# Performance work log

Hardware: AMD Instinct MI355X
Metric: run time of the kernel (lower is better)

Reference implementation:

```python
import jax, jax.numpy as jnp
import numpy as np

N_NODES = 100000
N_EDGES = 1600000
EPS = 1e-5
ALPHA = 0.01  # leaky relu slope


def gcn_conv(x, src, dst, W, b, n_nodes):
    """PyG GCNConv: h = W x, add self-loops, out = D^-1/2 (A+I) D^-1/2 h + b."""
    h = x @ W  # [N, d_out]
    # add self loops
    loop = jnp.arange(n_nodes, dtype=src.dtype)
    s = jnp.concatenate([src, loop])
    d = jnp.concatenate([dst, loop])
    # symmetric normalization: deg computed at destination over A + I
    deg = jax.ops.segment_sum(jnp.ones_like(d, dtype=h.dtype), d, num_segments=n_nodes)
    dinv = jnp.where(deg > 0, jax.lax.rsqrt(deg), 0.0)
    norm = dinv[s] * dinv[d]  # [E+N]
    msg = h[s] * norm[:, None]  # gather + scale (memory bound)
    out = jax.ops.segment_sum(msg, d, num_segments=n_nodes)
    return out + b


def batch_norm(x, gamma, beta):
    mu = jnp.mean(x, axis=0)
    var = jnp.var(x, axis=0)
    return (x - mu) * jax.lax.rsqrt(var + EPS) * gamma + beta


def setup_inputs() -> dict:
    key = jax.random.key(0)
    ks = jax.random.split(key, 6)
    emb = jax.random.normal(ks[0], (N_NODES, 64), dtype=jnp.float32)
    edge_index = jax.random.randint(ks[1], (2, N_EDGES), 0, N_NODES, dtype=jnp.int32)
    W1 = jax.random.normal(ks[2], (64, 128), dtype=jnp.float32) * 0.05
    W2 = jax.random.normal(ks[3], (128, 256), dtype=jnp.float32) * 0.05
    Wf = jax.random.normal(ks[4], (256, 256), dtype=jnp.float32) * 0.05
    return {
        "embeddings": emb, "edge_index": edge_index,
        "W1": W1, "b1": jnp.zeros((128,), jnp.float32),
        "g1": jnp.ones((128,), jnp.float32), "beta1": jnp.zeros((128,), jnp.float32),
        "W2": W2, "b2": jnp.zeros((256,), jnp.float32),
        "g2": jnp.ones((256,), jnp.float32), "beta2": jnp.zeros((256,), jnp.float32),
        "Wf": Wf, "bf": jnp.zeros((256,), jnp.float32),
    }


def reference(embeddings, edge_index, W1, b1, g1, beta1, W2, b2, g2, beta2, Wf, bf):
    src, dst = edge_index[0], edge_index[1]
    x = gcn_conv(embeddings, src, dst, W1, b1, N_NODES)
    x = batch_norm(x, g1, beta1)
    x = jnp.where(x >= 0, x, ALPHA * x)  # leaky relu; dropout = identity (eval)
    x = gcn_conv(x, src, dst, W2, b2, N_NODES)
    x = batch_norm(x, g2, beta2)
    x = jnp.where(x >= 0, x, ALPHA * x)
    return x @ Wf + bf
```

## Files before the change

### kernel.cpp

```cpp
#include <hip/hip_runtime.h>

#define NN 100000
#define NE 1600000
constexpr float EPS_BN = 1e-5f;
constexpr float ALPHA = 0.01f;
constexpr int GBN = 128;
constexpr int NBUCK = (NN + 127) / 128;
constexpr int GA = 128;
constexpr int EPB = NE / GA;

typedef __attribute__((ext_vector_type(8))) short short8;
typedef __attribute__((ext_vector_type(4))) float f32x4;

__device__ __forceinline__ float bfu2f(uint lo16) {
    union { uint i; float f; } v; v.i = lo16 << 16; return v.f;
}
__device__ __forceinline__ float bfhi2f(uint u) {
    union { uint i; float f; } v; v.i = u & 0xffff0000u; return v.f;
}
__device__ __forceinline__ ushort f2bf(float f) {
    union { float f; uint i; } v; v.f = f;
    return (ushort)((v.i + 0x7fffu + ((v.i >> 16) & 1u)) >> 16);
}

__global__ __launch_bounds__(256) void k_bhist(const int* __restrict__ dstv, int* __restrict__ bcnt) {
    __shared__ int hist[NBUCK];
    for (int i = threadIdx.x; i < NBUCK; i += 256) hist[i] = 0;
    __syncthreads();
    int base = blockIdx.x * EPB;
    for (int i = threadIdx.x; i < EPB; i += 256)
        atomicAdd(&hist[dstv[base + i] >> 7], 1);
    __syncthreads();
    for (int i = threadIdx.x; i < NBUCK; i += 256)
        bcnt[blockIdx.x * NBUCK + i] = hist[i];
}

__global__ __launch_bounds__(1024) void k_bscan(const int* __restrict__ bcnt,
                                                int* __restrict__ gcur, int* __restrict__ bbase) {
    __shared__ int tot[1024];
    int b = threadIdx.x;
    int t = 0;
    if (b < NBUCK)
        for (int k = 0; k < GA; ++k) t += bcnt[k * NBUCK + b];
    tot[b] = t;
    __syncthreads();
    for (int off = 1; off < 1024; off <<= 1) {
        int u = (b >= off) ? tot[b - off] : 0;
        __syncthreads();
        tot[b] += u;
        __syncthreads();
    }
    int ex = tot[b] - t;
    if (b < NBUCK) {
        bbase[b] = ex;
        int cur = ex;
        for (int k = 0; k < GA; ++k) { gcur[k * NBUCK + b] = cur; cur += bcnt[k * NBUCK + b]; }
    }
    if (b == 0) bbase[NBUCK] = NE;
}

__global__ __launch_bounds__(256) void k_bscatter(const int* __restrict__ srcv, const int* __restrict__ dstv,
                                                  const int* __restrict__ gcur, uint* __restrict__ bpair) {
    __shared__ int lcur[NBUCK];
    for (int i = threadIdx.x; i < NBUCK; i += 256) lcur[i] = gcur[blockIdx.x * NBUCK + i];
    __syncthreads();
    int base = blockIdx.x * EPB;
    for (int i = threadIdx.x; i < EPB; i += 256) {
        int d = dstv[base + i], s = srcv[base + i];
        int slot = atomicAdd(&lcur[d >> 7], 1);
        bpair[slot] = ((uint)(d & 127) << 17) | (uint)s;
    }
}

__global__ __launch_bounds__(256) void k_bcsr(const uint* __restrict__ bpair, const int* __restrict__ bbase,
                                              int* __restrict__ col, int* __restrict__ cnt,
                                              int* __restrict__ indptr, float* __restrict__ dinv) {
    __shared__ int h[128];
    __shared__ int off[128];
    int b = blockIdx.x, t = threadIdx.x;
    int p0 = bbase[b], p1 = bbase[b + 1];
    if (t < 128) h[t] = 0;
    __syncthreads();
    for (int i = p0 + t; i < p1; i += 256)
        atomicAdd(&h[bpair[i] >> 17], 1);
    __syncthreads();
    if (t < 128) off[t] = h[t];
    __syncthreads();
    for (int o = 1; o < 128; o <<= 1) {
        int u = 0;
        if (t < 128 && t >= o) u = off[t - o];
        __syncthreads();
        if (t < 128) off[t] += u;
        __syncthreads();
    }
    if (t < 128) {
        int st = p0 + off[t] - h[t];
        int node = b * 128 + t;
        if (node < NN) {
            indptr[node] = st;
            cnt[node] = h[t];
            dinv[node] = rsqrtf((float)(h[t] + 1));
        }
        off[t] = st;
    }
    __syncthreads();
    for (int i = p0 + t; i < p1; i += 256) {
        uint u = bpair[i];
        int slot = atomicAdd(&off[u >> 17], 1);
        col[slot] = (int)(u & 0x1FFFFu);
    }
}

__global__ void k_wtrans_all(const float* __restrict__ W1, const float* __restrict__ W2,
                             const float* __restrict__ Wf, ushort* __restrict__ w1t,
                             ushort* __restrict__ w2t, ushort* __restrict__ wft) {
    int i = blockIdx.x * 256 + threadIdx.x;
    if (i < 8192) {
        int m = i / 64, k = i % 64;
        w1t[i] = f2bf(W1[(size_t)k * 128 + m]);
    } else if (i < 8192 + 32768) {
        int j = i - 8192;
        int m = j / 128, k = j % 128;
        w2t[j] = f2bf(W2[(size_t)k * 256 + m]);
    } else if (i < 8192 + 32768 + 65536) {
        int j = i - 8192 - 32768;
        int m = j / 256, k = j % 256;
        wft[j] = f2bf(Wf[(size_t)k * 256 + m]);
    }
}

__global__ __launch_bounds__(256) void k_semb(const float* __restrict__ emb, const float* __restrict__ dinv,
                                              uint2* __restrict__ embs) {
    int i = blockIdx.x * 256 + threadIdx.x;
    if (i >= NN * 16) return;
    int row = i >> 4;
    float dn = dinv[row];
    float4 f = ((const float4*)emb)[i];
    uint2 o;
    o.x = (uint)f2bf(f.x * dn) | ((uint)f2bf(f.y * dn) << 16);
    o.y = (uint)f2bf(f.z * dn) | ((uint)f2bf(f.w * dn) << 16);
    embs[i] = o;
}

__global__ __launch_bounds__(256) void k_x2s(const ushort* __restrict__ H1, const float* __restrict__ sc,
                                             const float* __restrict__ sh, const float* __restrict__ dinv,
                                             ushort* __restrict__ x2s) {
    int i = blockIdx.x * 256 + threadIdx.x;
    if (i >= NN * 16) return;
    int row = i >> 4, f0 = (i & 15) * 8;
    float dn = dinv[row];
    uint4 u = ((const uint4*)H1)[i];
    uint uu[4] = {u.x, u.y, u.z, u.w};
    uint oo[4];
#pragma unroll
    for (int q = 0; q < 4; ++q) {
        int f = f0 + q * 2;
        float e0 = bfu2f(uu[q] & 0xffffu) * sc[f] + sh[f];
        float e1 = bfhi2f(uu[q]) * sc[f + 1] + sh[f + 1];
        e0 = ((e0 >= 0.f) ? e0 : ALPHA * e0) * dn;
        e1 = ((e1 >= 0.f) ? e1 : ALPHA * e1) * dn;
        oo[q] = (uint)f2bf(e0) | ((uint)f2bf(e1) << 16);
    }
    uint4 o; o.x = oo[0]; o.y = oo[1]; o.z = oo[2]; o.w = oo[3];
    ((uint4*)x2s)[i] = o;
}

__global__ __launch_bounds__(64) void k_agg64(const ushort* __restrict__ X, const int* __restrict__ indptr,
                                              const int* __restrict__ cnt, const int* __restrict__ col,
                                              const float* __restrict__ dinv, ushort* __restrict__ out) {
    int n = blockIdx.x, t = threadIdx.x;
    int t2 = t & 31, h = t >> 5;
    __shared__ int sc[64];
    int start = indptr[n], c = cnt[n];
    const uint* Xu = (const uint*)X;
    float a0 = 0.f, a1 = 0.f;
    if (h == 0) {
        uint u = Xu[(size_t)n * 32 + t2];
        a0 = bfu2f(u & 0xffffu); a1 = bfhi2f(u);
    }
    for (int base = 0; base < c; base += 64) {
        int m = min(64, c - base);
        if (t < m) sc[t] = col[start + base + t];
        __syncthreads();
#pragma unroll 2
        for (int j = h; j < m; j += 2) {
            uint v = Xu[(size_t)sc[j] * 32 + t2];
            a0 += bfu2f(v & 0xffffu); a1 += bfhi2f(v);
        }
        __syncthreads();
    }
    a0 += __shfl_xor(a0, 32);
    a1 += __shfl_xor(a1, 32);
    if (h == 0) {
        float dn = dinv[n];
        ((uint*)out)[(size_t)n * 32 + t2] = (uint)f2bf(a0 * dn) | ((uint)f2bf(a1 * dn) << 16);
    }
}

__global__ __launch_bounds__(64) void k_agg128(const ushort* __restrict__ X, const int* __restrict__ indptr,
                                               const int* __restrict__ cnt, const int* __restrict__ col,
                                               const float* __restrict__ dinv, ushort* __restrict__ out) {
    int n = blockIdx.x, t = threadIdx.x;
    __shared__ int sc[64];
    int start = indptr[n], c = cnt[n];
    const uint* Xu = (const uint*)X;
    uint u = Xu[(size_t)n * 64 + t];
    float a0 = bfu2f(u & 0xffffu), a1 = bfhi2f(u);
    float b0 = 0.f, b1 = 0.f;
    for (int base = 0; base < c; base += 64) {
        int m = min(64, c - base);
        if (t < m) sc[t] = col[start + base + t];
        __syncthreads();
        int j = 0;
#pragma unroll 2
        for (; j + 2 <= m; j += 2) {
            uint v0 = Xu[(size_t)sc[j] * 64 + t];
            uint v1 = Xu[(size_t)sc[j + 1] * 64 + t];
            a0 += bfu2f(v0 & 0xffffu); a1 += bfhi2f(v0);
            b0 += bfu2f(v1 & 0xffffu); b1 += bfhi2f(v1);
        }
        if (j < m) {
            uint v = Xu[(size_t)sc[j] * 64 + t];
            a0 += bfu2f(v & 0xffffu); a1 += bfhi2f(v);
        }
        __syncthreads();
    }
    a0 += b0; a1 += b1;
    float dn = dinv[n];
    ((uint*)out)[(size_t)n * 64 + t] = (uint)f2bf(a0 * dn) | ((uint)f2bf(a1 * dn) << 16);
}

template <int AT>
__device__ __forceinline__ uint4 xform8(uint4 u, int kbase, const float* s_sc, const float* s_sh) {
    if constexpr (AT == 1) {
        uint uu[4] = {u.x, u.y, u.z, u.w};
        uint oo[4];
#pragma unroll
        for (int q = 0; q < 4; ++q) {
            int kq = kbase + q * 2;
            float e0 = bfu2f(uu[q] & 0xffffu) * s_sc[kq] + s_sh[kq];
            float e1 = bfhi2f(uu[q]) * s_sc[kq + 1] + s_sh[kq + 1];
            e0 = (e0 >= 0.f) ? e0 : ALPHA * e0;
            e1 = (e1 >= 0.f) ? e1 : ALPHA * e1;
            oo[q] = (uint)f2bf(e0) | ((uint)f2bf(e1) << 16);
        }
        return make_uint4(oo[0], oo[1], oo[2], oo[3]);
    } else {
        return u;
    }
}

template <int K, int NOUT, int AT, int OUT>
__global__ __launch_bounds__(256) void k_mgemm(
        const void* __restrict__ Ap, const ushort* __restrict__ BT, void* __restrict__ Cp,
        const float* __restrict__ scale, const float* __restrict__ shift,
        const float* __restrict__ bias) {
    constexpr int BM = 64, BK = 32, LDA = 40;
    constexpr int WN = NOUT / 4;
    constexpr int NF = WN / 16;
    constexpr int NT = K / BK;
    __shared__ ushort As[2][BM * LDA];
    __shared__ float s_sc[K];
    __shared__ float s_sh[K];

    int tid = threadIdx.x;
    int brow = blockIdx.x * BM;
    int lane = tid & 63, wid = tid >> 6;
    int fr = lane & 15, fq = lane >> 4;
    int fk = fq * 8;

    const int srow = tid >> 2, sk0 = (tid & 3) * 8;
    const int grow = brow + srow;
    const bool aok = grow < NN;
    const ushort* arp = (const ushort*)Ap + (size_t)grow * K + sk0;

    if constexpr (AT == 1) {
        for (int i = tid; i < K; i += 256) { s_sc[i] = scale[i]; s_sh[i] = shift[i]; }
        __syncthreads();
    }

    f32x4 acc[4][NF];
#pragma unroll
    for (int mi = 0; mi < 4; ++mi)
#pragma unroll
        for (int ni = 0; ni < NF; ++ni) acc[mi][ni] = (f32x4){0.f, 0.f, 0.f, 0.f};

    uint4 av = make_uint4(0, 0, 0, 0);
    if (aok) av = *(const uint4*)arp;
    av = xform8<AT>(av, sk0, s_sc, s_sh);
    *(uint4*)&As[0][srow * LDA + sk0] = av;

    for (int t = 0; t < NT; ++t) {
        __syncthreads();
        uint4 anext = make_uint4(0, 0, 0, 0);
        if (t + 1 < NT && aok)
            anext = *(const uint4*)(arp + (t + 1) * BK);

        short8 bfv[NF];
#pragma unroll
        for (int ni = 0; ni < NF; ++ni)
            bfv[ni] = *(const short8*)(BT + (size_t)(wid * WN + ni * 16 + fr) * K + t * BK + fk);

        short8 af[4];
#pragma unroll
        for (int mi = 0; mi < 4; ++mi)
            af[mi] = *(const short8*)&As[t & 1][(mi * 16 + fr) * LDA + fk];

#pragma unroll
        for (int mi = 0; mi < 4; ++mi)
#pragma unroll
            for (int ni = 0; ni < NF; ++ni)
                acc[mi][ni] = __builtin_amdgcn_mfma_f32_16x16x32_bf16(af[mi], bfv[ni], acc[mi][ni], 0, 0, 0);

        if (t + 1 < NT) {
            anext = xform8<AT>(anext, (t + 1) * BK + sk0, s_sc, s_sh);
            *(uint4*)&As[(t + 1) & 1][srow * LDA + sk0] = anext;
        }
    }

    float bv[NF];
#pragma unroll
    for (int ni = 0; ni < NF; ++ni) bv[ni] = bias[wid * WN + ni * 16 + fr];

    if constexpr (OUT == 1) {
        float* outf = (float*)Cp;
#pragma unroll
        for (int mi = 0; mi < 4; ++mi)
#pragma unroll
            for (int r = 0; r < 4; ++r) {
                int row = brow + mi * 16 + fq * 4 + r;
                if (row < NN) {
#pragma unroll
                    for (int ni = 0; ni < NF; ++ni) {
                        int c = wid * WN + ni * 16 + fr;
                        outf[(size_t)row * NOUT + c] = acc[mi][ni][r] + bv[ni];
                    }
                }
            }
    } else {
        ushort* outb = (ushort*)Cp;
#pragma unroll
        for (int mi = 0; mi < 4; ++mi)
#pragma unroll
            for (int r = 0; r < 4; ++r) {
                int row = brow + mi * 16 + fq * 4 + r;
                if (row < NN) {
#pragma unroll
                    for (int ni = 0; ni < NF; ++ni) {
                        int c = wid * WN + ni * 16 + fr;
                        outb[(size_t)row * NOUT + c] = f2bf(acc[mi][ni][r] + bv[ni]);
                    }
                }
            }
    }
}

template <int M>
__global__ __launch_bounds__(256) void k_bnpart(const ushort* __restrict__ X, float* __restrict__ partials) {
    constexpr int FG = M / 8, RP = 256 / FG;
    __shared__ float rs[RP * M];
    __shared__ float rq[RP * M];
    int fg = threadIdx.x % FG, r0 = threadIdx.x / FG;
    float s[8] = {0, 0, 0, 0, 0, 0, 0, 0}, q[8] = {0, 0, 0, 0, 0, 0, 0, 0};
    for (int n = blockIdx.x * RP + r0; n < NN; n += GBN * RP) {
        uint4 u = ((const uint4*)X)[(size_t)n * FG + fg];
        uint uu[4] = {u.x, u.y, u.z, u.w};
#pragma unroll
        for (int p = 0; p < 4; ++p) {
            float v0 = bfu2f(uu[p] & 0xffffu), v1 = bfhi2f(uu[p]);
            s[p * 2] += v0; q[p * 2] += v0 * v0;
            s[p * 2 + 1] += v1; q[p * 2 + 1] += v1 * v1;
        }
    }
    int f0 = fg * 8;
#pragma unroll
    for (int j = 0; j < 8; ++j) {
        rs[r0 * M + f0 + j] = s[j];
        rq[r0 * M + f0 + j] = q[j];
    }
    __syncthreads();
    for (int h = RP / 2; h; h >>= 1) {
        if (r0 < h) {
#pragma unroll
            for (int j = 0; j < 8; ++j) {
                rs[r0 * M + f0 + j] += rs[(r0 + h) * M + f0 + j];
                rq[r0 * M + f0 + j] += rq[(r0 + h) * M + f0 + j];
            }
        }
        __syncthreads();
    }
    if (threadIdx.x < M) {
        partials[(size_t)blockIdx.x * 2 * M + threadIdx.x] = rs[threadIdx.x];
        partials[(size_t)blockIdx.x * 2 * M + M + threadIdx.x] = rq[threadIdx.x];
    }
}

template <int M>
__global__ void k_bnred(const float* __restrict__ partials, const float* __restrict__ g,
                        const float* __restrict__ be, float* __restrict__ scale,
                        float* __restrict__ shift) {
    int f = threadIdx.x;
    if (f < M) {
        float s = 0.f, q = 0.f;
        for (int b = 0; b < GBN; ++b) {
            s += partials[(size_t)b * 2 * M + f];
            q += partials[(size_t)b * 2 * M + M + f];
        }
        float mu = s * (1.f / NN);
        float var = q * (1.f / NN) - mu * mu;
        float r = rsqrtf(var + EPS_BN);
        float sc = g[f] * r;
        scale[f] = sc;
        shift[f] = be[f] - mu * sc;
    }
}

extern "C" void kernel_launch(void* const* d_in, const int* in_sizes, int n_in,
                              void* d_out, int out_size, void* d_ws, size_t ws_size,
                              hipStream_t stream) {
    const float* emb = (const float*)d_in[0];
    const int* eidx  = (const int*)d_in[1];
    const float* W1  = (const float*)d_in[2];
    const float* b1  = (const float*)d_in[3];
    const float* g1  = (const float*)d_in[4];
    const float* be1 = (const float*)d_in[5];
    const float* W2  = (const float*)d_in[6];
    const float* b2  = (const float*)d_in[7];
    const float* g2  = (const float*)d_in[8];
    const float* be2 = (const float*)d_in[9];
    const float* Wf  = (const float*)d_in[10];
    const float* bf  = (const float*)d_in[11];
    float* out = (float*)d_out;
    const int* srcv = eidx;
    const int* dstv = eidx + NE;

    char* w = (char*)d_ws;
    auto alloc = [&](size_t bytes) {
        char* p = w;
        w += (bytes + 255) / 256 * 256;
        return p;
    };
    int* cnt    = (int*)alloc((size_t)NN * 4);
    int* indptr = (int*)alloc((size_t)NN * 4);
    int* bcnt   = (int*)alloc((size_t)NBUCK * GA * 4);
    int* gcur   = (int*)alloc((size_t)NBUCK * GA * 4);
    int* bbase  = (int*)alloc((size_t)(NBUCK + 1) * 4);
    int* colb   = (int*)alloc((size_t)NE * 4);
    uint* bpair = (uint*)alloc((size_t)NE * 4);
    float* dinv = (float*)alloc((size_t)NN * 4);
    float* partials = (float*)alloc((size_t)GBN * 512 * 4);
    float* sc1 = (float*)alloc(128 * 4);
    float* sh1 = (float*)alloc(128 * 4);
    float* sc2 = (float*)alloc(256 * 4);
    float* sh2 = (float*)alloc(256 * 4);
    ushort* w1t = (ushort*)alloc((size_t)128 * 64 * 2);
    ushort* w2t = (ushort*)alloc((size_t)256 * 128 * 2);
    ushort* wft = (ushort*)alloc((size_t)256 * 256 * 2);
    ushort* slabA = (ushort*)alloc((size_t)NN * 128 * 2);
    ushort* slabB = (ushort*)alloc((size_t)NN * 128 * 2);
    ushort* H2 = (ushort*)alloc((size_t)NN * 256 * 2);

    ushort* embs = slabA;
    ushort* aggE = slabB;
    ushort* H1   = slabA;
    ushort* x2s  = slabB;
    ushort* agg2 = slabA;

    k_bhist<<<GA, 256, 0, stream>>>(dstv, bcnt);
    k_bscan<<<1, 1024, 0, stream>>>(bcnt, gcur, bbase);
    k_bscatter<<<GA, 256, 0, stream>>>(srcv, dstv, gcur, bpair);
    k_bcsr<<<NBUCK, 256, 0, stream>>>(bpair, bbase, colb, cnt, indptr, dinv);

    k_wtrans_all<<<(8192 + 32768 + 65536 + 255) / 256, 256, 0, stream>>>(W1, W2, Wf, w1t, w2t, wft);

    constexpr int GX = (NN + 63) / 64;

    k_semb<<<(NN * 16 + 255) / 256, 256, 0, stream>>>(emb, dinv, (uint2*)embs);
    k_agg64<<<NN, 64, 0, stream>>>(embs, indptr, cnt, colb, dinv, aggE);
    k_mgemm<64, 128, 2, 2><<<GX, 256, 0, stream>>>(aggE, w1t, H1, nullptr, nullptr, b1);
    k_bnpart<128><<<GBN, 256, 0, stream>>>(H1, partials);
    k_bnred<128><<<1, 256, 0, stream>>>(partials, g1, be1, sc1, sh1);

    k_x2s<<<(NN * 16 + 255) / 256, 256, 0, stream>>>(H1, sc1, sh1, dinv, x2s);
    k_agg128<<<NN, 64, 0, stream>>>(x2s, indptr, cnt, colb, dinv, agg2);
    k_mgemm<128, 256, 2, 2><<<GX, 256, 0, stream>>>(agg2, w2t, H2, nullptr, nullptr, b2);
    k_bnpart<256><<<GBN, 256, 0, stream>>>(H2, partials);
    k_bnred<256><<<1, 256, 0, stream>>>(partials, g2, be2, sc2, sh2);

    k_mgemm<256, 256, 1, 1><<<GX, 256, 0, stream>>>(H2, wft, out, sc2, sh2, bf);
}
```

Before: 364.3 us.

## Fuse batch-norm statistics into GEMM epilogue and parallelize bucket scan

The GEMM epilogue now accumulates per-column sum and sum-of-squares and writes per-block partials, which removes the separate k_bnpart passes that re-read H1 and H2. The final reduction now runs across 8 or 16 blocks instead of a single block. The single-block bucket scan is split into a parallel totals kernel, a small scan and a parallel cursor kernel. Statistics are now taken from fp32 values before bf16 rounding, which slightly changes numerics, and the change adds kernel launches.

```diff
diff --git a/kernel.cpp b/kernel.cpp
--- a/kernel.cpp
+++ b/kernel.cpp
@@ -4,10 +4,10 @@
 #define NE 1600000
 constexpr float EPS_BN = 1e-5f;
 constexpr float ALPHA = 0.01f;
-constexpr int GBN = 128;
 constexpr int NBUCK = (NN + 127) / 128;
 constexpr int GA = 128;
 constexpr int EPB = NE / GA;
+constexpr int GX = (NN + 63) / 64;
 
 typedef __attribute__((ext_vector_type(8))) short short8;
 typedef __attribute__((ext_vector_type(4))) float f32x4;
@@ -35,28 +35,38 @@
         bcnt[blockIdx.x * NBUCK + i] = hist[i];
 }
 
-__global__ __launch_bounds__(1024) void k_bscan(const int* __restrict__ bcnt,
-                                                int* __restrict__ gcur, int* __restrict__ bbase) {
-    __shared__ int tot[1024];
+__global__ __launch_bounds__(256) void k_btot(const int* __restrict__ bcnt, int* __restrict__ tot) {
+    int b = blockIdx.x * 256 + threadIdx.x;
+    if (b < NBUCK) {
+        int t = 0;
+        for (int k = 0; k < GA; ++k) t += bcnt[k * NBUCK + b];
+        tot[b] = t;
+    }
+}
+
+__global__ __launch_bounds__(1024) void k_bscanT(const int* __restrict__ tot, int* __restrict__ bbase) {
+    __shared__ int tmp[1024];
     int b = threadIdx.x;
-    int t = 0;
-    if (b < NBUCK)
-        for (int k = 0; k < GA; ++k) t += bcnt[k * NBUCK + b];
-    tot[b] = t;
+    int v = (b < NBUCK) ? tot[b] : 0;
+    tmp[b] = v;
     __syncthreads();
     for (int off = 1; off < 1024; off <<= 1) {
-        int u = (b >= off) ? tot[b - off] : 0;
-        __syncthreads();
-        tot[b] += u;
-        __syncthreads();
-    }
-    int ex = tot[b] - t;
+        int u = (b >= off) ? tmp[b - off] : 0;
+        __syncthreads();
+        tmp[b] += u;
+        __syncthreads();
+    }
+    if (b < NBUCK) bbase[b] = tmp[b] - v;
+    if (b == 0) bbase[NBUCK] = NE;
+}
+
+__global__ __launch_bounds__(256) void k_bcur(const int* __restrict__ bcnt, const int* __restrict__ bbase,
+                                              int* __restrict__ gcur) {
+    int b = blockIdx.x * 256 + threadIdx.x;
     if (b < NBUCK) {
-        bbase[b] = ex;
-        int cur = ex;
+        int cur = bbase[b];
         for (int k = 0; k < GA; ++k) { gcur[k * NBUCK + b] = cur; cur += bcnt[k * NBUCK + b]; }
     }
-    if (b == 0) bbase[NBUCK] = NE;
 }
 
 __global__ __launch_bounds__(256) void k_bscatter(const int* __restrict__ srcv, const int* __restrict__ dstv,
@@ -250,11 +260,11 @@
     }
 }
 
-template <int K, int NOUT, int AT, int OUT>
+template <int K, int NOUT, int AT, int OUT, bool STATS>
 __global__ __launch_bounds__(256) void k_mgemm(
         const void* __restrict__ Ap, const ushort* __restrict__ BT, void* __restrict__ Cp,
         const float* __restrict__ scale, const float* __restrict__ shift,
-        const float* __restrict__ bias) {
+        const float* __restrict__ bias, float* __restrict__ partials) {
     constexpr int BM = 64, BK = 32, LDA = 40;
     constexpr int WN = NOUT / 4;
     constexpr int NF = WN / 16;
@@ -322,92 +332,70 @@
 #pragma unroll
     for (int ni = 0; ni < NF; ++ni) bv[ni] = bias[wid * WN + ni * 16 + fr];
 
-    if constexpr (OUT == 1) {
-        float* outf = (float*)Cp;
-#pragma unroll
-        for (int mi = 0; mi < 4; ++mi)
-#pragma unroll
-            for (int r = 0; r < 4; ++r) {
-                int row = brow + mi * 16 + fq * 4 + r;
-                if (row < NN) {
-#pragma unroll
-                    for (int ni = 0; ni < NF; ++ni) {
-                        int c = wid * WN + ni * 16 + fr;
-                        outf[(size_t)row * NOUT + c] = acc[mi][ni][r] + bv[ni];
-                    }
+    float sv[NF], qv[NF];
+#pragma unroll
+    for (int ni = 0; ni < NF; ++ni) { sv[ni] = 0.f; qv[ni] = 0.f; }
+
+#pragma unroll
+    for (int mi = 0; mi < 4; ++mi)
+#pragma unroll
+        for (int r = 0; r < 4; ++r) {
+            int row = brow + mi * 16 + fq * 4 + r;
+            if (row < NN) {
+#pragma unroll
+                for (int ni = 0; ni < NF; ++ni) {
+                    float x = acc[mi][ni][r] + bv[ni];
+                    int c = wid * WN + ni * 16 + fr;
+                    if constexpr (OUT == 1)
+                        ((float*)Cp)[(size_t)row * NOUT + c] = x;
+                    else
+                        ((ushort*)Cp)[(size_t)row * NOUT + c] = f2bf(x);
+                    if constexpr (STATS) { sv[ni] += x; qv[ni] += x * x; }
                 }
             }
-    } else {
-        ushort* outb = (ushort*)Cp;
-#pragma unroll
-        for (int mi = 0; mi < 4; ++mi)
-#pragma unroll
-            for (int r = 0; r < 4; ++r) {
-                int row = brow + mi * 16 + fq * 4 + r;
-                if (row < NN) {
-#pragma unroll
-                    for (int ni = 0; ni < NF; ++ni) {
-                        int c = wid * WN + ni * 16 + fr;
-                        outb[(size_t)row * NOUT + c] = f2bf(acc[mi][ni][r] + bv[ni]);
-                    }
-                }
+        }
+
+    if constexpr (STATS) {
+#pragma unroll
+        for (int ni = 0; ni < NF; ++ni) {
+            sv[ni] += __shfl_down(sv[ni], 32); qv[ni] += __shfl_down(qv[ni], 32);
+            sv[ni] += __shfl_down(sv[ni], 16); qv[ni] += __shfl_down(qv[ni], 16);
+        }
+        if (fq == 0) {
+            float* pb = partials + (size_t)blockIdx.x * 2 * NOUT;
+#pragma unroll
+            for (int ni = 0; ni < NF; ++ni) {
+                int c = wid * WN + ni * 16 + fr;
+                pb[c] = sv[ni];
+                pb[NOUT + c] = qv[ni];
             }
+        }
     }
 }
 
 template <int M>
-__global__ __launch_bounds__(256) void k_bnpart(const ushort* __restrict__ X, float* __restrict__ partials) {
-    constexpr int FG = M / 8, RP = 256 / FG;
-    __shared__ float rs[RP * M];
-    __shared__ float rq[RP * M];
-    int fg = threadIdx.x % FG, r0 = threadIdx.x / FG;
-    float s[8] = {0, 0, 0, 0, 0, 0, 0, 0}, q[8] = {0, 0, 0, 0, 0, 0, 0, 0};
-    for (int n = blockIdx.x * RP + r0; n < NN; n += GBN * RP) {
-        uint4 u = ((const uint4*)X)[(size_t)n * FG + fg];
-        uint uu[4] = {u.x, u.y, u.z, u.w};
-#pragma unroll
-        for (int p = 0; p < 4; ++p) {
-            float v0 = bfu2f(uu[p] & 0xffffu), v1 = bfhi2f(uu[p]);
-            s[p * 2] += v0; q[p * 2] += v0 * v0;
-            s[p * 2 + 1] += v1; q[p * 2 + 1] += v1 * v1;
-        }
-    }
-    int f0 = fg * 8;
-#pragma unroll
-    for (int j = 0; j < 8; ++j) {
-        rs[r0 * M + f0 + j] = s[j];
-        rq[r0 * M + f0 + j] = q[j];
-    }
-    __syncthreads();
-    for (int h = RP / 2; h; h >>= 1) {
-        if (r0 < h) {
-#pragma unroll
-            for (int j = 0; j < 8; ++j) {
-                rs[r0 * M + f0 + j] += rs[(r0 + h) * M + f0 + j];
-                rq[r0 * M + f0 + j] += rq[(r0 + h) * M + f0 + j];
-            }
-        }
-        __syncthreads();
-    }
-    if (threadIdx.x < M) {
-        partials[(size_t)blockIdx.x * 2 * M + threadIdx.x] = rs[threadIdx.x];
-        partials[(size_t)blockIdx.x * 2 * M + M + threadIdx.x] = rq[threadIdx.x];
-    }
-}
-
-template <int M>
-__global__ void k_bnred(const float* __restrict__ partials, const float* __restrict__ g,
-                        const float* __restrict__ be, float* __restrict__ scale,
-                        float* __restrict__ shift) {
-    int f = threadIdx.x;
-    if (f < M) {
-        float s = 0.f, q = 0.f;
-        for (int b = 0; b < GBN; ++b) {
-            s += partials[(size_t)b * 2 * M + f];
-            q += partials[(size_t)b * 2 * M + M + f];
-        }
-        float mu = s * (1.f / NN);
-        float var = q * (1.f / NN) - mu * mu;
+__global__ __launch_bounds__(256) void k_bnred(const float* __restrict__ partials, const float* __restrict__ g,
+                                               const float* __restrict__ be, float* __restrict__ scale,
+                                               float* __restrict__ shift) {
+    int tid = threadIdx.x;
+    int fl = tid & 15, bl = tid >> 4;
+    int f = blockIdx.x * 16 + fl;
+    float s = 0.f, q = 0.f;
+    for (int b = bl; b < GX; b += 16) {
+        s += partials[(size_t)b * 2 * M + f];
+        q += partials[(size_t)b * 2 * M + M + f];
+    }
+    __shared__ float rs[256], rq[256];
+    rs[tid] = s; rq[tid] = q;
+    __syncthreads();
+    for (int h = 128; h >= 16; h >>= 1) {
+        if (tid < h) { rs[tid] += rs[tid + h]; rq[tid] += rq[tid + h]; }
+        __syncthreads();
+    }
+    if (tid < 16) {
+        float su = rs[tid], qu = rq[tid];
+        float mu = su * (1.f / NN);
+        float var = qu * (1.f / NN) - mu * mu;
         float r = rsqrtf(var + EPS_BN);
         float sc = g[f] * r;
         scale[f] = sc;
@@ -444,11 +432,12 @@
     int* indptr = (int*)alloc((size_t)NN * 4);
     int* bcnt   = (int*)alloc((size_t)NBUCK * GA * 4);
     int* gcur   = (int*)alloc((size_t)NBUCK * GA * 4);
+    int* tot    = (int*)alloc((size_t)NBUCK * 4);
     int* bbase  = (int*)alloc((size_t)(NBUCK + 1) * 4);
     int* colb   = (int*)alloc((size_t)NE * 4);
     uint* bpair = (uint*)alloc((size_t)NE * 4);
     float* dinv = (float*)alloc((size_t)NN * 4);
-    float* partials = (float*)alloc((size_t)GBN * 512 * 4);
+    float* partials = (float*)alloc((size_t)GX * 512 * 4);
     float* sc1 = (float*)alloc(128 * 4);
     float* sh1 = (float*)alloc(128 * 4);
     float* sc2 = (float*)alloc(256 * 4);
@@ -466,26 +455,26 @@
     ushort* x2s  = slabB;
     ushort* agg2 = slabA;
 
+    constexpr int GB4 = (NBUCK + 255) / 256;
+
     k_bhist<<<GA, 256, 0, stream>>>(dstv, bcnt);
-    k_bscan<<<1, 1024, 0, stream>>>(bcnt, gcur, bbase);
+    k_btot<<<GB4, 256, 0, stream>>>(bcnt, tot);
+    k_bscanT<<<1, 1024, 0, stream>>>(tot, bbase);
+    k_bcur<<<GB4, 256, 0, stream>>>(bcnt, bbase, gcur);
     k_bscatter<<<GA, 256, 0, stream>>>(srcv, dstv, gcur, bpair);
     k_bcsr<<<NBUCK, 256, 0, stream>>>(bpair, bbase, colb, cnt, indptr, dinv);
 
     k_wtrans_all<<<(8192 + 32768 + 65536 + 255) / 256, 256, 0, stream>>>(W1, W2, Wf, w1t, w2t, wft);
 
-    constexpr int GX = (NN + 63) / 64;
-
     k_semb<<<(NN * 16 + 255) / 256, 256, 0, stream>>>(emb, dinv, (uint2*)embs);
     k_agg64<<<NN, 64, 0, stream>>>(embs, indptr, cnt, colb, dinv, aggE);
-    k_mgemm<64, 128, 2, 2><<<GX, 256, 0, stream>>>(aggE, w1t, H1, nullptr, nullptr, b1);
-    k_bnpart<128><<<GBN, 256, 0, stream>>>(H1, partials);
-    k_bnred<128><<<1, 256, 0, stream>>>(partials, g1, be1, sc1, sh1);
+    k_mgemm<64, 128, 2, 2, true><<<GX, 256, 0, stream>>>(aggE, w1t, H1, nullptr, nullptr, b1, partials);
+    k_bnred<128><<<8, 256, 0, stream>>>(partials, g1, be1, sc1, sh1);
 
     k_x2s<<<(NN * 16 + 255) / 256, 256, 0, stream>>>(H1, sc1, sh1, dinv, x2s);
     k_agg128<<<NN, 64, 0, stream>>>(x2s, indptr, cnt, colb, dinv, agg2);
-    k_mgemm<128, 256, 2, 2><<<GX, 256, 0, stream>>>(agg2, w2t, H2, nullptr, nullptr, b2);
-    k_bnpart<256><<<GBN, 256, 0, stream>>>(H2, partials);
-    k_bnred<256><<<1, 256, 0, stream>>>(partials, g2, be2, sc2, sh2);
-
-    k_mgemm<256, 256, 1, 1><<<GX, 256, 0, stream>>>(H2, wft, out, sc2, sh2, bf);
-}
+    k_mgemm<128, 256, 2, 2, true><<<GX, 256, 0, stream>>>(agg2, w2t, H2, nullptr, nullptr, b2, partials);
+    k_bnred<256><<<16, 256, 0, stream>>>(partials, g2, be2, sc2, sh2);
+
+    k_mgemm<256, 256, 1, 1, false><<<GX, 256, 0, stream>>>(H2, wft, out, sc2, sh2, bf, nullptr);
+}
```

Measured after the change: 349.5 us. 4.1% less time.
